# Optimization experiments

Hardware: AMD Instinct MI355X
Metric: run time of the kernel (lower is better)

The kernel has to match this reference:

```python
import jax, jax.numpy as jnp
import numpy as np
import math

D_MODEL = 1024
N_HEADS = 16
D_FF = 4096
D_K = D_MODEL // N_HEADS
B, S = 2, 2048
EPS = 1e-5


def _linear_params(key, fan_in, fan_out):
    kw, kb = jax.random.split(key)
    bound = 1.0 / math.sqrt(fan_in)
    W = jax.random.uniform(kw, (fan_out, fan_in), jnp.float32, -bound, bound)
    b = jax.random.uniform(kb, (fan_out,), jnp.float32, -bound, bound)
    return W, b


def setup_inputs() -> dict:
    key = jax.random.key(0)
    ks = jax.random.split(key, 8)
    x = jax.random.normal(ks[0], (B, S, D_MODEL), jnp.float32)
    # causal mask, broadcast over batch and heads; 0 -> masked
    mask = jnp.tril(jnp.ones((S, S), jnp.int32))[None, None, :, :]
    wq, bq = _linear_params(ks[1], D_MODEL, D_MODEL)
    wk, bk = _linear_params(ks[2], D_MODEL, D_MODEL)
    wv, bv = _linear_params(ks[3], D_MODEL, D_MODEL)
    wo, bo = _linear_params(ks[4], D_MODEL, D_MODEL)
    w1, b1 = _linear_params(ks[5], D_MODEL, D_FF)
    w2, b2 = _linear_params(ks[6], D_FF, D_MODEL)
    g1 = jnp.ones((D_MODEL,), jnp.float32)
    be1 = jnp.zeros((D_MODEL,), jnp.float32)
    g2 = jnp.ones((D_MODEL,), jnp.float32)
    be2 = jnp.zeros((D_MODEL,), jnp.float32)
    return dict(x=x, mask=mask, wq=wq, bq=bq, wk=wk, bk=bk, wv=wv, bv=bv,
                wo=wo, bo=bo, w1=w1, b1=b1, w2=w2, b2=b2,
                g1=g1, be1=be1, g2=g2, be2=be2)


def _layernorm(x, g, b):
    mu = jnp.mean(x, axis=-1, keepdims=True)
    var = jnp.mean(jnp.square(x - mu), axis=-1, keepdims=True)
    return (x - mu) * jax.lax.rsqrt(var + EPS) * g + b


def reference(x, mask, wq, bq, wk, bk, wv, bv, wo, bo, w1, b1, w2, b2, g1, be1, g2, be2):
    Bsz, Sl, _ = x.shape
    def heads(t):  # [B,S,D] -> [B,H,S,d_k]
        return t.reshape(Bsz, Sl, N_HEADS, D_K).transpose(0, 2, 1, 3)
    Q = heads(x @ wq.T + bq)
    K = heads(x @ wk.T + bk)
    V = heads(x @ wv.T + bv)
    scores = jnp.einsum('bhqd,bhkd->bhqk', Q, K) / math.sqrt(D_K)
    scores = jnp.where(mask == 0, jnp.float32(-1e9), scores)
    attn = jax.nn.softmax(scores, axis=-1)
    out = jnp.einsum('bhqk,bhkd->bhqd', attn, V)
    out = out.transpose(0, 2, 1, 3).reshape(Bsz, Sl, D_MODEL)
    attn_out = out @ wo.T + bo
    h = _layernorm(x + attn_out, g1, be1)  # dropout is identity in eval
    ff = jax.nn.relu(h @ w1.T + b1) @ w2.T + b2
    return _layernorm(h + ff, g2, be2)
```

## Files before the change

kernel.cpp:

```cpp
#include <hip/hip_runtime.h>
#include <hip/hip_bf16.h>


using f32x4 = __attribute__((ext_vector_type(4))) float;
using s16x8 = __attribute__((ext_vector_type(8))) short;

constexpr int D_MODEL = 1024;
constexpr int D_FF    = 4096;
constexpr int DK      = 64;
constexpr int BB      = 2;
constexpr int SS      = 2048;
constexpr int NTOK    = BB * SS;

#define QSCALE 0.18033688011112042f

__device__ __forceinline__ ushort f2bf(float f) {
    unsigned u = __float_as_uint(f);
    u += 0x7fffu + ((u >> 16) & 1u);
    return (ushort)(u >> 16);
}

__device__ __forceinline__ float bflo(uint v) { return __uint_as_float(v << 16); }
__device__ __forceinline__ float bfhi(uint v) { return __uint_as_float(v & 0xffff0000u); }

__device__ __forceinline__ float ex2(float x) {
    float r;
    asm("v_exp_f32 %0, %1" : "=v"(r) : "v"(x));
    return r;
}

__device__ __forceinline__ void gload_lds16(const void* g, void* l) {
    __builtin_amdgcn_global_load_lds(
        (const __attribute__((address_space(1))) void*)g,
        (__attribute__((address_space(3))) void*)l, 16, 0, 0);
}

__device__ __forceinline__ void wait_vm4() {
    asm volatile("s_waitcnt vmcnt(4)" ::: "memory");
    __builtin_amdgcn_sched_barrier(0);
}
__device__ __forceinline__ void wait_vm0() {
    asm volatile("s_waitcnt vmcnt(0)" ::: "memory");
    __builtin_amdgcn_sched_barrier(0);
}
__device__ __forceinline__ void wait_lgkm0() {
    asm volatile("s_waitcnt lgkmcnt(0)" ::: "memory");
    __builtin_amdgcn_sched_barrier(0);
}

struct CvtArgs { const float* src[7]; ushort* dst[7]; };

__global__ __launch_bounds__(256) void cvt_all(CvtArgs a) {
    constexpr long S[8] = {0L<<20, 1L<<20, 2L<<20, 3L<<20,
                           4L<<20, 8L<<20, 12L<<20, 16L<<20};
    long i = ((long)blockIdx.x * 256 + threadIdx.x) * 4;
    int s = 0;
#pragma unroll
    for (int j = 1; j < 7; ++j) if (i >= S[j]) s = j;
    long off = i - S[s];
    float4 v = *(const float4*)(a.src[s] + off);
    ushort4 o;
    o.x = f2bf(v.x); o.y = f2bf(v.y); o.z = f2bf(v.z); o.w = f2bf(v.w);
    *(ushort4*)(a.dst[s] + off) = o;
}

__global__ __launch_bounds__(512, 2) void gemm256_relu(
        const ushort* __restrict__ A, const ushort* __restrict__ Wt,
        const float* __restrict__ bias, ushort* __restrict__ C,
        int M, int N, int K) {
    __shared__ __align__(16) char Als[2][2][128 * 128];
    __shared__ __align__(16) char Bls[2][2][128 * 128];

    const int nwg = (int)gridDim.x;
    const int id  = (int)blockIdx.x;
    const int sw  = (id & 7) * (nwg >> 3) + (id >> 3);
    const int gx  = N >> 8;
    const int bx  = sw % gx, by = sw / gx;
    const int bm0 = by << 8, bn0 = bx << 8;

    const int t  = threadIdx.x;
    const int l  = t & 63;
    const int w  = t >> 6;
    const int li = l & 15, g = l >> 4;
    const int wm = w >> 2, wn = w & 3;

    const int srow  = w * 8 + (l >> 3);
    const int scolb = (l & 7) * 16;
    const int svz   = (scolb ^ ((srow & 7) << 4)) >> 1;
    const int nk    = K >> 6;

    auto stA = [&](int buf, int half, int kt) {
        if (kt >= nk) return;
        const ushort* src = A + (size_t)(bm0 + half * 128 + srow) * K + kt * 64 + svz;
        char* dst = Als[buf][half] + w * 1024;
        gload_lds16(src, dst);
        gload_lds16(src + (size_t)64 * K, dst + 8192);
    };
    auto stB = [&](int buf, int half, int kt) {
        if (kt >= nk) return;
        const ushort* src = Wt + (size_t)(bn0 + half * 128 + srow) * K + kt * 64 + svz;
        char* dst = Bls[buf][half] + w * 1024;
        gload_lds16(src, dst);
        gload_lds16(src + (size_t)64 * K, dst + 8192);
    };

    const int rdsw = (li & 7) << 4;

    f32x4 acc[8][4];
#pragma unroll
    for (int m = 0; m < 8; ++m)
#pragma unroll
        for (int n = 0; n < 4; ++n)
            acc[m][n] = (f32x4){0.f, 0.f, 0.f, 0.f};

    auto ldA2 = [&](int buf, int q, s16x8 af[2][2]) {
#pragma unroll
        for (int m2 = 0; m2 < 2; ++m2)
#pragma unroll
            for (int kk = 0; kk < 2; ++kk)
                af[m2][kk] = *(const s16x8*)(Als[buf][wm] +
                    ((q * 2 + m2) * 16 + li) * 128 + ((kk * 64 + g * 16) ^ rdsw));
    };
    auto ldB8 = [&](int buf, s16x8 bfr[4][2]) {
#pragma unroll
        for (int nf = 0; nf < 4; ++nf)
#pragma unroll
            for (int kk = 0; kk < 2; ++kk)
                bfr[nf][kk] = *(const s16x8*)(Bls[buf][wn >> 1] +
                    ((wn & 1) * 64 + nf * 16 + li) * 128 + ((kk * 64 + g * 16) ^ rdsw));
    };
    auto mfmaq = [&](int q, s16x8 af[2][2], s16x8 bfr[4][2], int wm_mode) {
        __builtin_amdgcn_s_barrier();
        wait_lgkm0();
        __builtin_amdgcn_s_setprio(1);
#pragma unroll
        for (int m2 = 0; m2 < 2; ++m2)
#pragma unroll
            for (int nf = 0; nf < 4; ++nf)
#pragma unroll
            for (int kk = 0; kk < 2; ++kk)
                acc[q * 2 + m2][nf] = __builtin_amdgcn_mfma_f32_16x16x32_bf16(
                    af[m2][kk], bfr[nf][kk], acc[q * 2 + m2][nf], 0, 0, 0);
        __builtin_amdgcn_s_setprio(0);
        if (wm_mode == 4) wait_vm4();
        else if (wm_mode == 0) wait_vm0();
        __builtin_amdgcn_s_barrier();
    };

    stB(0, 0, 0); stB(0, 1, 0);
    stA(0, 0, 0); stA(0, 1, 0);
    stB(1, 0, 1); stB(1, 1, 1);
    wait_vm4();
    __builtin_amdgcn_s_barrier();

    const int ni = nk >> 1;
    for (int i = 0; i < ni; ++i) {
        const int t0 = 2 * i;
        const bool last = (i == ni - 1);
        {
            s16x8 bfr[4][2];
            { ldB8(0, bfr); s16x8 af[2][2]; ldA2(0, 0, af);
              stA(1, 0, t0 + 1);                      mfmaq(0, af, bfr, -1); }
            { s16x8 af[2][2]; ldA2(0, 1, af);
              stA(1, 1, t0 + 1); stB(0, 0, t0 + 2);   mfmaq(1, af, bfr, -1); }
            { s16x8 af[2][2]; ldA2(0, 2, af);
              stB(0, 1, t0 + 2);                      mfmaq(2, af, bfr, -1); }
            { s16x8 af[2][2]; ldA2(0, 3, af);
                                                      mfmaq(3, af, bfr, last ? 0 : 4); }
        }
        {
            s16x8 bfr[4][2];
            { ldB8(1, bfr); s16x8 af[2][2]; ldA2(1, 0, af);
              stA(0, 0, t0 + 2);                      mfmaq(0, af, bfr, -1); }
            { s16x8 af[2][2]; ldA2(1, 1, af);
              stA(0, 1, t0 + 2);                      mfmaq(1, af, bfr, -1); }
            { s16x8 af[2][2]; ldA2(1, 2, af);
              stB(1, 0, t0 + 3);                      mfmaq(2, af, bfr, -1); }
            { s16x8 af[2][2]; ldA2(1, 3, af);
              stB(1, 1, t0 + 3);
                                                      mfmaq(3, af, bfr, last ? -1 : 4); }
        }
    }

#pragma unroll
    for (int mf = 0; mf < 8; ++mf) {
        int row0 = bm0 + wm * 128 + mf * 16 + g * 4;
#pragma unroll
        for (int nf = 0; nf < 4; ++nf) {
            int col = bn0 + wn * 64 + nf * 16 + li;
            float bsv = bias[col];
#pragma unroll
            for (int r = 0; r < 4; ++r) {
                float v = fmaxf(acc[mf][nf][r] + bsv, 0.f);
                C[(size_t)(row0 + r) * N + col] = f2bf(v);
            }
        }
    }
}

__global__ __launch_bounds__(512, 2) void gemm256_qkvt(
        const ushort* __restrict__ xb, const ushort* __restrict__ wqkb,
        const ushort* __restrict__ wvb,
        const float* __restrict__ bq, const float* __restrict__ bk,
        const float* __restrict__ bv,
        ushort* __restrict__ QKb, ushort* __restrict__ VtG) {
    __shared__ __align__(16) char Als[2][2][128 * 128];
    __shared__ __align__(16) char Bls[2][2][128 * 128];

    const int id = (int)blockIdx.x;
    const int sw = (id & 7) * 24 + (id >> 3);
    const bool vt = (sw >= 128);
    const ushort *Aop, *Wop;
    int bm0, bn0;
    if (!vt) { bm0 = (sw >> 3) << 8;  bn0 = (sw & 7) << 8;          Aop = xb;  Wop = wqkb; }
    else     { int s2 = sw - 128; bm0 = (s2 >> 4) << 8; bn0 = (s2 & 15) << 8; Aop = wvb; Wop = xb; }

    const int t  = threadIdx.x;
    const int l  = t & 63;
    const int w  = t >> 6;
    const int li = l & 15, g = l >> 4;
    const int wm = w >> 2, wn = w & 3;

    const int srow  = w * 8 + (l >> 3);
    const int scolb = (l & 7) * 16;
    const int svz   = (scolb ^ ((srow & 7) << 4)) >> 1;
    constexpr int K = 1024, nk = 16;

    auto stA = [&](int buf, int half, int kt) {
        if (kt >= nk) return;
        const ushort* src = Aop + (size_t)(bm0 + half * 128 + srow) * K + kt * 64 + svz;
        char* dst = Als[buf][half] + w * 1024;
        gload_lds16(src, dst);
        gload_lds16(src + (size_t)64 * K, dst + 8192);
    };
    auto stB = [&](int buf, int half, int kt) {
        if (kt >= nk) return;
        const ushort* src = Wop + (size_t)(bn0 + half * 128 + srow) * K + kt * 64 + svz;
        char* dst = Bls[buf][half] + w * 1024;
        gload_lds16(src, dst);
        gload_lds16(src + (size_t)64 * K, dst + 8192);
    };

    const int rdsw = (li & 7) << 4;

    f32x4 acc[8][4];
#pragma unroll
    for (int m = 0; m < 8; ++m)
#pragma unroll
        for (int n = 0; n < 4; ++n)
            acc[m][n] = (f32x4){0.f, 0.f, 0.f, 0.f};

    auto ldA2 = [&](int buf, int q, s16x8 af[2][2]) {
#pragma unroll
        for (int m2 = 0; m2 < 2; ++m2)
#pragma unroll
            for (int kk = 0; kk < 2; ++kk)
                af[m2][kk] = *(const s16x8*)(Als[buf][wm] +
                    ((q * 2 + m2) * 16 + li) * 128 + ((kk * 64 + g * 16) ^ rdsw));
    };
    auto ldB8 = [&](int buf, s16x8 bfr[4][2]) {
#pragma unroll
        for (int nf = 0; nf < 4; ++nf)
#pragma unroll
            for (int kk = 0; kk < 2; ++kk)
                bfr[nf][kk] = *(const s16x8*)(Bls[buf][wn >> 1] +
                    ((wn & 1) * 64 + nf * 16 + li) * 128 + ((kk * 64 + g * 16) ^ rdsw));
    };
    auto mfmaq = [&](int q, s16x8 af[2][2], s16x8 bfr[4][2], int wm_mode) {
        __builtin_amdgcn_s_barrier();
        wait_lgkm0();
        __builtin_amdgcn_s_setprio(1);
#pragma unroll
        for (int m2 = 0; m2 < 2; ++m2)
#pragma unroll
            for (int nf = 0; nf < 4; ++nf)
#pragma unroll
            for (int kk = 0; kk < 2; ++kk)
                acc[q * 2 + m2][nf] = __builtin_amdgcn_mfma_f32_16x16x32_bf16(
                    af[m2][kk], bfr[nf][kk], acc[q * 2 + m2][nf], 0, 0, 0);
        __builtin_amdgcn_s_setprio(0);
        if (wm_mode == 4) wait_vm4();
        else if (wm_mode == 0) wait_vm0();
        __builtin_amdgcn_s_barrier();
    };

    stB(0, 0, 0); stB(0, 1, 0);
    stA(0, 0, 0); stA(0, 1, 0);
    stB(1, 0, 1); stB(1, 1, 1);
    wait_vm4();
    __builtin_amdgcn_s_barrier();

    const int ni = nk >> 1;
    for (int i = 0; i < ni; ++i) {
        const int t0 = 2 * i;
        const bool last = (i == ni - 1);
        {
            s16x8 bfr[4][2];
            { ldB8(0, bfr); s16x8 af[2][2]; ldA2(0, 0, af);
              stA(1, 0, t0 + 1);                      mfmaq(0, af, bfr, -1); }
            { s16x8 af[2][2]; ldA2(0, 1, af);
              stA(1, 1, t0 + 1); stB(0, 0, t0 + 2);   mfmaq(1, af, bfr, -1); }
            { s16x8 af[2][2]; ldA2(0, 2, af);
              stB(0, 1, t0 + 2);                      mfmaq(2, af, bfr, -1); }
            { s16x8 af[2][2]; ldA2(0, 3, af);
                                                      mfmaq(3, af, bfr, last ? 0 : 4); }
        }
        {
            s16x8 bfr[4][2];
            { ldB8(1, bfr); s16x8 af[2][2]; ldA2(1, 0, af);
              stA(0, 0, t0 + 2);                      mfmaq(0, af, bfr, -1); }
            { s16x8 af[2][2]; ldA2(1, 1, af);
              stA(0, 1, t0 + 2);                      mfmaq(1, af, bfr, -1); }
            { s16x8 af[2][2]; ldA2(1, 2, af);
              stB(1, 0, t0 + 3);                      mfmaq(2, af, bfr, -1); }
            { s16x8 af[2][2]; ldA2(1, 3, af);
              stB(1, 1, t0 + 3);
                                                      mfmaq(3, af, bfr, last ? -1 : 4); }
        }
    }

#pragma unroll
    for (int mf = 0; mf < 8; ++mf) {
        int row0 = bm0 + wm * 128 + mf * 16 + g * 4;
#pragma unroll
        for (int nf = 0; nf < 4; ++nf) {
            int col = bn0 + wn * 64 + nf * 16 + li;
            if (!vt) {
                float bsv = (col < 1024) ? bq[col] : bk[col - 1024];
                float sc  = (col < 1024) ? QSCALE : 1.f;
#pragma unroll
                for (int r = 0; r < 4; ++r) {
                    float v = (acc[mf][nf][r] + bsv) * sc;
                    QKb[(size_t)(row0 + r) * 2048 + col] = f2bf(v);
                }
            } else {
#pragma unroll
                for (int r = 0; r < 4; ++r) {
                    float v = acc[mf][nf][r] + bv[row0 + r];
                    VtG[(size_t)(row0 + r) * 4096 + col] = f2bf(v);
                }
            }
        }
    }
}

__global__ __launch_bounds__(256, 2) void gemm_bt(
        const ushort* __restrict__ A, const ushort* __restrict__ W,
        const float* __restrict__ bias,
        ushort* __restrict__ Cout, int M, int N, int Klen, int ldk, int gx, int splitk) {
    __shared__ __align__(16) char Asb[2][128 * 128];
    __shared__ __align__(16) char Bsb[2][128 * 128];

    const int nwg = (int)gridDim.x;
    const int id  = (int)blockIdx.x;
    const int sw  = (id & 7) * (nwg >> 3) + (id >> 3);
    const int tps = nwg / splitk;
    const int s   = sw / tps;
    const int rem = sw - s * tps;
    const int bx  = rem % gx, by = rem / gx;

    const int t  = threadIdx.x;
    const int l  = t & 63;
    const int w  = t >> 6;
    const int wr = w >> 1, wc = w & 1;
    const int li = l & 15, g = l >> 4;
    const int bm0 = by << 7;
    const int bn0 = bx << 7;
    const int kbase = s * Klen;

    f32x4 acc[4][4];
#pragma unroll
    for (int m = 0; m < 4; ++m)
#pragma unroll
        for (int n = 0; n < 4; ++n)
            acc[m][n] = (f32x4){0.f, 0.f, 0.f, 0.f};

    const int rsub = l >> 3, slot = l & 7;
    const int swzel = (((slot * 16) ^ (rsub << 4)) >> 1);

    auto stage = [&](int buf, int k0) {
#pragma unroll
        for (int i = 0; i < 4; ++i) {
            const int rbase = i * 32 + w * 8;
            gload_lds16(A + (size_t)(bm0 + rbase + rsub) * ldk + kbase + k0 + swzel,
                        Asb[buf] + rbase * 128);
            gload_lds16(W + (size_t)(bn0 + rbase + rsub) * ldk + kbase + k0 + swzel,
                        Bsb[buf] + rbase * 128);
        }
    };

    const int nk = Klen >> 6;
    stage(0, 0);
    __syncthreads();

    for (int tt = 0; tt < nk; ++tt) {
        const int cur = tt & 1;
        if (tt + 1 < nk) stage(cur ^ 1, (tt + 1) << 6);
#pragma unroll
        for (int ks = 0; ks < 2; ++ks) {
            s16x8 af[4], bfr[4];
#pragma unroll
            for (int m = 0; m < 4; ++m) {
                int row = wr * 64 + m * 16 + li;
                af[m] = *(const s16x8*)(Asb[cur] + row * 128 + (((ks * 4 + g) * 16) ^ ((row & 7) << 4)));
            }
#pragma unroll
            for (int n = 0; n < 4; ++n) {
                int row = wc * 64 + n * 16 + li;
                bfr[n] = *(const s16x8*)(Bsb[cur] + row * 128 + (((ks * 4 + g) * 16) ^ ((row & 7) << 4)));
            }
            __builtin_amdgcn_s_setprio(1);
#pragma unroll
            for (int m = 0; m < 4; ++m)
#pragma unroll
                for (int n = 0; n < 4; ++n)
                    acc[m][n] = __builtin_amdgcn_mfma_f32_16x16x32_bf16(af[m], bfr[n], acc[m][n], 0, 0, 0);
            __builtin_amdgcn_s_setprio(0);
        }
        __syncthreads();
    }

    const bool dobias = (s == 0);
    ushort* Cb = Cout + (size_t)s * M * N;
#pragma unroll
    for (int m = 0; m < 4; ++m) {
        int row0 = bm0 + wr * 64 + m * 16 + g * 4;
#pragma unroll
        for (int n = 0; n < 4; ++n) {
            int col = bn0 + wc * 64 + n * 16 + li;
            float bsv = dobias ? bias[col] : 0.f;
#pragma unroll
            for (int r = 0; r < 4; ++r) {
                float v = acc[m][n][r] + bsv;
                Cb[(size_t)(row0 + r) * N + col] = f2bf(v);
            }
        }
    }
}

__global__ __launch_bounds__(256, 4) void attn_kernel(
        const ushort* __restrict__ QKb, const ushort* __restrict__ VtG,
        ushort* __restrict__ po, float* __restrict__ ml) {
    __shared__ __align__(16) char Ks[2][64 * 128];
    __shared__ __align__(16) char Vs[2][64 * 128];
    __shared__ __align__(16) char Ps[4][16 * 128];

    const int t  = threadIdx.x;
    const int l  = t & 63;
    const int w  = t >> 6;
    const int li = l & 15, g = l >> 4;

    const int id   = (int)blockIdx.x;
    const int xcd  = id & 7;
    const int rest = id >> 3;
    const int grp  = xcd + 8 * (rest >> 5);
    const int k32  = rest & 31;
    const int h    = grp >> 1;
    const int b    = grp & 1;
    const int bx   = k32 & 15;
    const int half = k32 >> 4;

    const ushort* Kp = QKb + (size_t)(b * SS) * 2048 + 1024 + h * DK;
    const ushort* Vp = VtG + (size_t)(h * DK) * NTOK + b * SS;

    const int rsub = l >> 3, slot = l & 7;
    const int swzsrc = (slot * 16) ^ (rsub << 4);

    auto stage = [&](int buf, int kt) {
#pragma unroll
        for (int c = 0; c < 2; ++c) {
            int row0 = (w + c * 4) * 8;
            gload_lds16((const char*)(Kp + (size_t)(kt + row0 + rsub) * 2048) + swzsrc,
                        Ks[buf] + row0 * 128);
            gload_lds16((const char*)(Vp + (size_t)(row0 + rsub) * NTOK + kt) + swzsrc,
                        Vs[buf] + row0 * 128);
        }
    };

    char* Pw = Ps[w];
    const int rswz = (li & 7) << 4;

    s16x8 vones;
#pragma unroll
    for (int j = 0; j < 8; ++j) vones[j] = (short)0x3F80;

    const int hi  = SS / 64 - 1 - bx;
    const int lo  = bx;
    const int qwH = hi * 64 + w * 16;
    const int qwL = lo * 64 + w * 16;

    s16x8 qfH[2], qfL[2];
    {
        const ushort* QpH = QKb + (size_t)(b * SS + qwH) * 2048 + h * DK;
        const ushort* QpL = QKb + (size_t)(b * SS + qwL) * 2048 + h * DK;
#pragma unroll
        for (int ds = 0; ds < 2; ++ds) {
            qfH[ds] = *(const s16x8*)(QpH + li * 2048 + ds * 32 + g * 8);
            qfL[ds] = *(const s16x8*)(QpL + li * 2048 + ds * 32 + g * 8);
        }
    }

    f32x4 oH[4], oL[4], osH, osL;
#pragma unroll
    for (int d = 0; d < 4; ++d) {
        oH[d] = (f32x4){0.f, 0.f, 0.f, 0.f};
        oL[d] = (f32x4){0.f, 0.f, 0.f, 0.f};
    }
    osH = (f32x4){0.f, 0.f, 0.f, 0.f};
    osL = (f32x4){0.f, 0.f, 0.f, 0.f};

    auto process = [&](const s16x8 (&qf)[2], f32x4 (&o)[4], f32x4& osum,
                       int j, int stripe, int qw, int cur) {
        const int kt = j * 64;
        f32x4 sa[4];
#pragma unroll
        for (int ks = 0; ks < 4; ++ks) sa[ks] = (f32x4){0.f, 0.f, 0.f, 0.f};
#pragma unroll
        for (int ks = 0; ks < 4; ++ks) {
            int row = ks * 16 + li;
#pragma unroll
            for (int ds = 0; ds < 2; ++ds) {
                s16x8 kf = *(const s16x8*)(Ks[cur] + row * 128 + ((ds * 64 + g * 16) ^ rswz));
                __builtin_amdgcn_s_setprio(1);
                sa[ks] = __builtin_amdgcn_mfma_f32_16x16x32_bf16(kf, qf[ds], sa[ks], 0, 0, 0);
                __builtin_amdgcn_s_setprio(0);
            }
        }

        const bool maskt = (j == stripe);
        float p[4][4];
#pragma unroll
        for (int ks = 0; ks < 4; ++ks)
#pragma unroll
            for (int r = 0; r < 4; ++r) {
                float sv = sa[ks][r];
                if (maskt && (kt + ks * 16 + g * 4 + r > qw + li)) sv = -1e30f;
                p[ks][r] = ex2(sv);
            }

#pragma unroll
        for (int ks = 0; ks < 4; ++ks) {
            uint u0, u1;
            asm("v_cvt_pk_bf16_f32 %0, %1, %2" : "=v"(u0) : "v"(p[ks][0]), "v"(p[ks][1]));
            asm("v_cvt_pk_bf16_f32 %0, %1, %2" : "=v"(u1) : "v"(p[ks][2]), "v"(p[ks][3]));
            uint2 uv; uv.x = u0; uv.y = u1;
            *(uint2*)(Pw + li * 128 + ((ks * 32 + g * 8) ^ rswz)) = uv;
        }

        s16x8 pf[2];
#pragma unroll
        for (int ks2 = 0; ks2 < 2; ++ks2)
            pf[ks2] = *(const s16x8*)(Pw + li * 128 + ((ks2 * 64 + g * 16) ^ rswz));
#pragma unroll
        for (int dblk = 0; dblk < 4; ++dblk) {
            int vrow = dblk * 16 + li;
#pragma unroll
            for (int ks2 = 0; ks2 < 2; ++ks2) {
                s16x8 vf = *(const s16x8*)(Vs[cur] + vrow * 128 + ((ks2 * 64 + g * 16) ^ rswz));
                __builtin_amdgcn_s_setprio(1);
                o[dblk] = __builtin_amdgcn_mfma_f32_16x16x32_bf16(pf[ks2], vf, o[dblk], 0, 0, 0);
                __builtin_amdgcn_s_setprio(0);
            }
        }
#pragma unroll
        for (int ks2 = 0; ks2 < 2; ++ks2)
            osum = __builtin_amdgcn_mfma_f32_16x16x32_bf16(pf[ks2], vones, osum, 0, 0, 0);
    };

    const int nt = ((hi - half) >> 1) + 1;
    stage(0, half * 64);
    __syncthreads();

    for (int it = 0; it < nt; ++it) {
        const int j   = half + 2 * it;
        const int cur = it & 1;
        if (it + 1 < nt) stage(cur ^ 1, j * 64 + 128);

        process(qfH, oH, osH, j, hi, qwH, cur);
        if (j <= lo)
            process(qfL, oL, osL, j, lo, qwL, cur);

        __syncthreads();
    }

#pragma unroll
    for (int r = 0; r < 4; ++r) {
        ushort* ppH = po + ((((size_t)(half * 2 + b)) * SS + qwH + g * 4 + r) * 16 + h) * 64;
        ushort* ppL = po + ((((size_t)(half * 2 + b)) * SS + qwL + g * 4 + r) * 16 + h) * 64;
#pragma unroll
        for (int dblk = 0; dblk < 4; ++dblk) {
            ppH[dblk * 16 + li] = f2bf(oH[dblk][r]);
            ppL[dblk * 16 + li] = f2bf(oL[dblk][r]);
        }
    }
    {
        const int qrow = l & 15;
        const int src  = (qrow >> 2) << 4;
        float tH0 = __shfl(osH[0], src), tH1 = __shfl(osH[1], src);
        float tH2 = __shfl(osH[2], src), tH3 = __shfl(osH[3], src);
        float tL0 = __shfl(osL[0], src), tL1 = __shfl(osL[1], src);
        float tL2 = __shfl(osL[2], src), tL3 = __shfl(osL[3], src);
        const int rr = qrow & 3;
        float lsH = rr == 0 ? tH0 : rr == 1 ? tH1 : rr == 2 ? tH2 : tH3;
        float lsL = rr == 0 ? tL0 : rr == 1 ? tL1 : rr == 2 ? tL2 : tL3;
        if (l < 16) {
            size_t mrowH = (((size_t)(half * 2 + b)) * SS + qwH + l) * 16 + h;
            ml[mrowH * 2]     = 0.f;
            ml[mrowH * 2 + 1] = lsH;
            size_t mrowL = (((size_t)(half * 2 + b)) * SS + qwL + l) * 16 + h;
            ml[mrowL * 2]     = 0.f;
            ml[mrowL * 2 + 1] = lsL;
        }
    }
}

__global__ __launch_bounds__(256) void attn_combine(
        const ushort* __restrict__ po, const float* __restrict__ ml,
        ushort* __restrict__ ctx) {
    const int idx = blockIdx.x * 256 + threadIdx.x;
    const int row = idx >> 4;
    const int d4  = (idx & 15) * 4;
    const int HR  = 2 * SS * 16;

    float m0 = ml[(size_t)row * 2],        l0 = ml[(size_t)row * 2 + 1];
    float m1 = ml[(size_t)(HR + row) * 2], l1 = ml[(size_t)(HR + row) * 2 + 1];
    float mx = fmaxf(m0, m1);
    float w0 = ex2(m0 - mx), w1 = ex2(m1 - mx);
    float inv = 1.0f / (l0 * w0 + l1 * w1);

    uint2 a = *(const uint2*)(po + (size_t)row * 64 + d4);
    uint2 c = *(const uint2*)(po + (size_t)(HR + row) * 64 + d4);
    float v0 = (bflo(a.x) * w0 + bflo(c.x) * w1) * inv;
    float v1 = (bfhi(a.x) * w0 + bfhi(c.x) * w1) * inv;
    float v2 = (bflo(a.y) * w0 + bflo(c.y) * w1) * inv;
    float v3 = (bfhi(a.y) * w0 + bfhi(c.y) * w1) * inv;
    ushort4 o;
    o.x = f2bf(v0); o.y = f2bf(v1); o.z = f2bf(v2); o.w = f2bf(v3);
    *(ushort4*)(ctx + (size_t)(row >> 4) * 1024 + (row & 15) * 64 + d4) = o;
}

template <bool WBF>
__global__ __launch_bounds__(256) void ln_fused(
        const float* __restrict__ xa, const ushort* __restrict__ pb,
        const float* __restrict__ gamma, const float* __restrict__ beta,
        float* __restrict__ outf, ushort* __restrict__ outb) {
    const int row = blockIdx.x;
    const int t   = threadIdx.x;
    const size_t off = (size_t)row * D_MODEL + t * 4;
    float4 a = *(const float4*)(xa + off);
    uint2 c = *(const uint2*)(pb + off);
    uint2 d = *(const uint2*)(pb + (size_t)NTOK * D_MODEL + off);
    float z0 = a.x + bflo(c.x) + bflo(d.x);
    float z1 = a.y + bfhi(c.x) + bfhi(d.x);
    float z2 = a.z + bflo(c.y) + bflo(d.y);
    float z3 = a.w + bfhi(c.y) + bfhi(d.y);
    float sum = z0 + z1 + z2 + z3;
    float sq  = z0 * z0 + z1 * z1 + z2 * z2 + z3 * z3;
#pragma unroll
    for (int o = 1; o < 64; o <<= 1) {
        sum += __shfl_xor(sum, o);
        sq  += __shfl_xor(sq, o);
    }
    __shared__ float s1[4], s2[4];
    if ((t & 63) == 0) { s1[t >> 6] = sum; s2[t >> 6] = sq; }
    __syncthreads();
    float tot = s1[0] + s1[1] + s1[2] + s1[3];
    float tsq = s2[0] + s2[1] + s2[2] + s2[3];
    const float invn = 1.0f / (float)D_MODEL;
    float mu  = tot * invn;
    float var = tsq * invn - mu * mu;
    float rstd = rsqrtf(var + 1e-5f);
    float4 gv = *(const float4*)(gamma + t * 4);
    float4 bv = *(const float4*)(beta + t * 4);
    float y0 = (z0 - mu) * rstd * gv.x + bv.x;
    float y1 = (z1 - mu) * rstd * gv.y + bv.y;
    float y2 = (z2 - mu) * rstd * gv.z + bv.z;
    float y3 = (z3 - mu) * rstd * gv.w + bv.w;
    float4 y = {y0, y1, y2, y3};
    *(float4*)(outf + off) = y;
    if constexpr (WBF) {
        ushort4 u;
        u.x = f2bf(y0); u.y = f2bf(y1); u.z = f2bf(y2); u.w = f2bf(y3);
        *(ushort4*)(outb + off) = u;
    }
}

extern "C" void kernel_launch(void* const* d_in, const int* in_sizes, int n_in,
                              void* d_out, int out_size, void* d_ws, size_t ws_size,
                              hipStream_t stream) {
    const float* x   = (const float*)d_in[0];
    const float* wq  = (const float*)d_in[2];  const float* bq  = (const float*)d_in[3];
    const float* wk  = (const float*)d_in[4];  const float* bk  = (const float*)d_in[5];
    const float* wv  = (const float*)d_in[6];  const float* bv  = (const float*)d_in[7];
    const float* wo  = (const float*)d_in[8];  const float* bo  = (const float*)d_in[9];
    const float* w1  = (const float*)d_in[10]; const float* b1  = (const float*)d_in[11];
    const float* w2  = (const float*)d_in[12]; const float* b2  = (const float*)d_in[13];
    const float* g1  = (const float*)d_in[14]; const float* be1 = (const float*)d_in[15];
    const float* g2  = (const float*)d_in[16]; const float* be2 = (const float*)d_in[17];
    float* out = (float*)d_out;

    char* ws = (char*)d_ws;
    const size_t MB = 1u << 20;
    ushort* wqkb = (ushort*)(ws + 0 * MB);
    ushort* wvb  = (ushort*)(ws + 4 * MB);
    ushort* wob  = (ushort*)(ws + 6 * MB);
    ushort* w1b  = (ushort*)(ws + 8 * MB);
    ushort* w2b  = (ushort*)(ws + 16 * MB);
    ushort* xb   = (ushort*)(ws + 24 * MB);
    ushort* QKb  = (ushort*)(ws + 32 * MB);
    ushort* VtG  = (ushort*)(ws + 48 * MB);
    ushort* ctx  = (ushort*)(ws + 56 * MB);
    ushort* po   = (ushort*)(ws + 64 * MB);
    float*  ml   = (float*)(ws + 81 * MB);
    ushort* p01  = (ushort*)(ws + 64 * MB);
    float*  h    = (float*)(ws + 96 * MB);
    ushort* hb   = (ushort*)(ws + 112 * MB);
    ushort* ffib = (ushort*)(ws + 24 * MB);

    CvtArgs ca;
    ca.src[0] = wq; ca.dst[0] = wqkb;
    ca.src[1] = wk; ca.dst[1] = wqkb + D_MODEL * D_MODEL;
    ca.src[2] = wv; ca.dst[2] = wvb;
    ca.src[3] = wo; ca.dst[3] = wob;
    ca.src[4] = w1; ca.dst[4] = w1b;
    ca.src[5] = w2; ca.dst[5] = w2b;
    ca.src[6] = x;  ca.dst[6] = xb;
    cvt_all<<<dim3(16384), dim3(256), 0, stream>>>(ca);

    gemm256_qkvt<<<dim3(192), dim3(512), 0, stream>>>(
        xb, wqkb, wvb, bq, bk, bv, QKb, VtG);

    attn_kernel<<<dim3(1024), dim3(256), 0, stream>>>(QKb, VtG, po, ml);
    attn_combine<<<dim3(4096), dim3(256), 0, stream>>>(po, ml, ctx);

    gemm_bt<<<dim3(512), dim3(256), 0, stream>>>(
        ctx, wob, bo, p01, NTOK, D_MODEL, 512, D_MODEL, 8, 2);
    ln_fused<true><<<dim3(NTOK), dim3(256), 0, stream>>>(x, p01, g1, be1, h, hb);

    gemm256_relu<<<dim3(256), dim3(512), 0, stream>>>(hb, w1b, b1, ffib, NTOK, D_FF, D_MODEL);

    gemm_bt<<<dim3(512), dim3(256), 0, stream>>>(
        ffib, w2b, b2, p01, NTOK, D_MODEL, 2048, D_FF, 8, 2);
    ln_fused<false><<<dim3(NTOK), dim3(256), 0, stream>>>(h, p01, g2, be2, out, nullptr);
}
```

Before: 213.1 us.

## Use pipelined 256x256 split-K GEMM for output and FFN-down projections

Replaces the 128x128 double-buffered gemm_bt with a generalized version of the 256x256, 512-thread software-pipelined GEMM already used for QKV. It now runs with split-K of 4, and the layernorm kernels sum four bf16 partial buffers instead of two. The larger tile with interleaved loads and MFMAs is meant to raise data reuse and keep the matrix units busier on the Wo and W2 projections. In exchange it doubles the partial-sum write and read traffic, which needs a workspace big enough for four partial buffers. The short K per split on the Wo GEMM also leaves little of the pipeline to work with.

```diff
diff --git a/kernel.cpp b/kernel.cpp
--- a/kernel.cpp
+++ b/kernel.cpp
@@ -198,22 +198,23 @@
     }
 }
 
-__global__ __launch_bounds__(512, 2) void gemm256_qkvt(
-        const ushort* __restrict__ xb, const ushort* __restrict__ wqkb,
-        const ushort* __restrict__ wvb,
-        const float* __restrict__ bq, const float* __restrict__ bk,
-        const float* __restrict__ bv,
-        ushort* __restrict__ QKb, ushort* __restrict__ VtG) {
+__global__ __launch_bounds__(512, 2) void gemm256_psum(
+        const ushort* __restrict__ A, const ushort* __restrict__ Wt,
+        const float* __restrict__ bias, ushort* __restrict__ Cout,
+        int M, int N, int Klen, int ldk, int splitk) {
     __shared__ __align__(16) char Als[2][2][128 * 128];
     __shared__ __align__(16) char Bls[2][2][128 * 128];
 
-    const int id = (int)blockIdx.x;
-    const int sw = (id & 7) * 24 + (id >> 3);
-    const bool vt = (sw >= 128);
-    const ushort *Aop, *Wop;
-    int bm0, bn0;
-    if (!vt) { bm0 = (sw >> 3) << 8;  bn0 = (sw & 7) << 8;          Aop = xb;  Wop = wqkb; }
-    else     { int s2 = sw - 128; bm0 = (s2 >> 4) << 8; bn0 = (s2 & 15) << 8; Aop = wvb; Wop = xb; }
+    const int nwg = (int)gridDim.x;
+    const int id  = (int)blockIdx.x;
+    const int sw  = (id & 7) * (nwg >> 3) + (id >> 3);
+    const int gx  = N >> 8;
+    const int tps = nwg / splitk;
+    const int s   = sw / tps;
+    const int rem = sw - s * tps;
+    const int bx  = rem % gx, by = rem / gx;
+    const int bm0 = by << 8, bn0 = bx << 8;
+    const int kbase = s * Klen;
 
     const int t  = threadIdx.x;
     const int l  = t & 63;
@@ -224,21 +225,21 @@
     const int srow  = w * 8 + (l >> 3);
     const int scolb = (l & 7) * 16;
     const int svz   = (scolb ^ ((srow & 7) << 4)) >> 1;
-    constexpr int K = 1024, nk = 16;
+    const int nk    = Klen >> 6;
 
     auto stA = [&](int buf, int half, int kt) {
         if (kt >= nk) return;
-        const ushort* src = Aop + (size_t)(bm0 + half * 128 + srow) * K + kt * 64 + svz;
+        const ushort* src = A + (size_t)(bm0 + half * 128 + srow) * ldk + kbase + kt * 64 + svz;
         char* dst = Als[buf][half] + w * 1024;
         gload_lds16(src, dst);
-        gload_lds16(src + (size_t)64 * K, dst + 8192);
+        gload_lds16(src + (size_t)64 * ldk, dst + 8192);
     };
     auto stB = [&](int buf, int half, int kt) {
         if (kt >= nk) return;
-        const ushort* src = Wop + (size_t)(bn0 + half * 128 + srow) * K + kt * 64 + svz;
+        const ushort* src = Wt + (size_t)(bn0 + half * 128 + srow) * ldk + kbase + kt * 64 + svz;
         char* dst = Bls[buf][half] + w * 1024;
         gload_lds16(src, dst);
-        gload_lds16(src + (size_t)64 * K, dst + 8192);
+        gload_lds16(src + (size_t)64 * ldk, dst + 8192);
     };
 
     const int rdsw = (li & 7) << 4;
@@ -319,6 +320,145 @@
         }
     }
 
+    const bool dobias = (s == 0);
+    ushort* Cb = Cout + (size_t)s * M * N;
+#pragma unroll
+    for (int mf = 0; mf < 8; ++mf) {
+        int row0 = bm0 + wm * 128 + mf * 16 + g * 4;
+#pragma unroll
+        for (int nf = 0; nf < 4; ++nf) {
+            int col = bn0 + wn * 64 + nf * 16 + li;
+            float bsv = dobias ? bias[col] : 0.f;
+#pragma unroll
+            for (int r = 0; r < 4; ++r) {
+                float v = acc[mf][nf][r] + bsv;
+                Cb[(size_t)(row0 + r) * N + col] = f2bf(v);
+            }
+        }
+    }
+}
+
+__global__ __launch_bounds__(512, 2) void gemm256_qkvt(
+        const ushort* __restrict__ xb, const ushort* __restrict__ wqkb,
+        const ushort* __restrict__ wvb,
+        const float* __restrict__ bq, const float* __restrict__ bk,
+        const float* __restrict__ bv,
+        ushort* __restrict__ QKb, ushort* __restrict__ VtG) {
+    __shared__ __align__(16) char Als[2][2][128 * 128];
+    __shared__ __align__(16) char Bls[2][2][128 * 128];
+
+    const int id = (int)blockIdx.x;
+    const int sw = (id & 7) * 24 + (id >> 3);
+    const bool vt = (sw >= 128);
+    const ushort *Aop, *Wop;
+    int bm0, bn0;
+    if (!vt) { bm0 = (sw >> 3) << 8;  bn0 = (sw & 7) << 8;          Aop = xb;  Wop = wqkb; }
+    else     { int s2 = sw - 128; bm0 = (s2 >> 4) << 8; bn0 = (s2 & 15) << 8; Aop = wvb; Wop = xb; }
+
+    const int t  = threadIdx.x;
+    const int l  = t & 63;
+    const int w  = t >> 6;
+    const int li = l & 15, g = l >> 4;
+    const int wm = w >> 2, wn = w & 3;
+
+    const int srow  = w * 8 + (l >> 3);
+    const int scolb = (l & 7) * 16;
+    const int svz   = (scolb ^ ((srow & 7) << 4)) >> 1;
+    constexpr int K = 1024, nk = 16;
+
+    auto stA = [&](int buf, int half, int kt) {
+        if (kt >= nk) return;
+        const ushort* src = Aop + (size_t)(bm0 + half * 128 + srow) * K + kt * 64 + svz;
+        char* dst = Als[buf][half] + w * 1024;
+        gload_lds16(src, dst);
+        gload_lds16(src + (size_t)64 * K, dst + 8192);
+    };
+    auto stB = [&](int buf, int half, int kt) {
+        if (kt >= nk) return;
+        const ushort* src = Wop + (size_t)(bn0 + half * 128 + srow) * K + kt * 64 + svz;
+        char* dst = Bls[buf][half] + w * 1024;
+        gload_lds16(src, dst);
+        gload_lds16(src + (size_t)64 * K, dst + 8192);
+    };
+
+    const int rdsw = (li & 7) << 4;
+
+    f32x4 acc[8][4];
+#pragma unroll
+    for (int m = 0; m < 8; ++m)
+#pragma unroll
+        for (int n = 0; n < 4; ++n)
+            acc[m][n] = (f32x4){0.f, 0.f, 0.f, 0.f};
+
+    auto ldA2 = [&](int buf, int q, s16x8 af[2][2]) {
+#pragma unroll
+        for (int m2 = 0; m2 < 2; ++m2)
+#pragma unroll
+            for (int kk = 0; kk < 2; ++kk)
+                af[m2][kk] = *(const s16x8*)(Als[buf][wm] +
+                    ((q * 2 + m2) * 16 + li) * 128 + ((kk * 64 + g * 16) ^ rdsw));
+    };
+    auto ldB8 = [&](int buf, s16x8 bfr[4][2]) {
+#pragma unroll
+        for (int nf = 0; nf < 4; ++nf)
+#pragma unroll
+            for (int kk = 0; kk < 2; ++kk)
+                bfr[nf][kk] = *(const s16x8*)(Bls[buf][wn >> 1] +
+                    ((wn & 1) * 64 + nf * 16 + li) * 128 + ((kk * 64 + g * 16) ^ rdsw));
+    };
+    auto mfmaq = [&](int q, s16x8 af[2][2], s16x8 bfr[4][2], int wm_mode) {
+        __builtin_amdgcn_s_barrier();
+        wait_lgkm0();
+        __builtin_amdgcn_s_setprio(1);
+#pragma unroll
+        for (int m2 = 0; m2 < 2; ++m2)
+#pragma unroll
+            for (int nf = 0; nf < 4; ++nf)
+#pragma unroll
+            for (int kk = 0; kk < 2; ++kk)
+                acc[q * 2 + m2][nf] = __builtin_amdgcn_mfma_f32_16x16x32_bf16(
+                    af[m2][kk], bfr[nf][kk], acc[q * 2 + m2][nf], 0, 0, 0);
+        __builtin_amdgcn_s_setprio(0);
+        if (wm_mode == 4) wait_vm4();
+        else if (wm_mode == 0) wait_vm0();
+        __builtin_amdgcn_s_barrier();
+    };
+
+    stB(0, 0, 0); stB(0, 1, 0);
+    stA(0, 0, 0); stA(0, 1, 0);
+    stB(1, 0, 1); stB(1, 1, 1);
+    wait_vm4();
+    __builtin_amdgcn_s_barrier();
+
+    const int ni = nk >> 1;
+    for (int i = 0; i < ni; ++i) {
+        const int t0 = 2 * i;
+        const bool last = (i == ni - 1);
+        {
+            s16x8 bfr[4][2];
+            { ldB8(0, bfr); s16x8 af[2][2]; ldA2(0, 0, af);
+              stA(1, 0, t0 + 1);                      mfmaq(0, af, bfr, -1); }
+            { s16x8 af[2][2]; ldA2(0, 1, af);
+              stA(1, 1, t0 + 1); stB(0, 0, t0 + 2);   mfmaq(1, af, bfr, -1); }
+            { s16x8 af[2][2]; ldA2(0, 2, af);
+              stB(0, 1, t0 + 2);                      mfmaq(2, af, bfr, -1); }
+            { s16x8 af[2][2]; ldA2(0, 3, af);
+                                                      mfmaq(3, af, bfr, last ? 0 : 4); }
+        }
+        {
+            s16x8 bfr[4][2];
+            { ldB8(1, bfr); s16x8 af[2][2]; ldA2(1, 0, af);
+              stA(0, 0, t0 + 2);                      mfmaq(0, af, bfr, -1); }
+            { s16x8 af[2][2]; ldA2(1, 1, af);
+              stA(0, 1, t0 + 2);                      mfmaq(1, af, bfr, -1); }
+            { s16x8 af[2][2]; ldA2(1, 2, af);
+              stB(1, 0, t0 + 3);                      mfmaq(2, af, bfr, -1); }
+            { s16x8 af[2][2]; ldA2(1, 3, af);
+              stB(1, 1, t0 + 3);
+                                                      mfmaq(3, af, bfr, last ? -1 : 4); }
+        }
+    }
+
 #pragma unroll
     for (int mf = 0; mf < 8; ++mf) {
         int row0 = bm0 + wm * 128 + mf * 16 + g * 4;
@@ -339,100 +479,6 @@
                     float v = acc[mf][nf][r] + bv[row0 + r];
                     VtG[(size_t)(row0 + r) * 4096 + col] = f2bf(v);
                 }
-            }
-        }
-    }
-}
-
-__global__ __launch_bounds__(256, 2) void gemm_bt(
-        const ushort* __restrict__ A, const ushort* __restrict__ W,
-        const float* __restrict__ bias,
-        ushort* __restrict__ Cout, int M, int N, int Klen, int ldk, int gx, int splitk) {
-    __shared__ __align__(16) char Asb[2][128 * 128];
-    __shared__ __align__(16) char Bsb[2][128 * 128];
-
-    const int nwg = (int)gridDim.x;
-    const int id  = (int)blockIdx.x;
-    const int sw  = (id & 7) * (nwg >> 3) + (id >> 3);
-    const int tps = nwg / splitk;
-    const int s   = sw / tps;
-    const int rem = sw - s * tps;
-    const int bx  = rem % gx, by = rem / gx;
-
-    const int t  = threadIdx.x;
-    const int l  = t & 63;
-    const int w  = t >> 6;
-    const int wr = w >> 1, wc = w & 1;
-    const int li = l & 15, g = l >> 4;
-    const int bm0 = by << 7;
-    const int bn0 = bx << 7;
-    const int kbase = s * Klen;
-
-    f32x4 acc[4][4];
-#pragma unroll
-    for (int m = 0; m < 4; ++m)
-#pragma unroll
-        for (int n = 0; n < 4; ++n)
-            acc[m][n] = (f32x4){0.f, 0.f, 0.f, 0.f};
-
-    const int rsub = l >> 3, slot = l & 7;
-    const int swzel = (((slot * 16) ^ (rsub << 4)) >> 1);
-
-    auto stage = [&](int buf, int k0) {
-#pragma unroll
-        for (int i = 0; i < 4; ++i) {
-            const int rbase = i * 32 + w * 8;
-            gload_lds16(A + (size_t)(bm0 + rbase + rsub) * ldk + kbase + k0 + swzel,
-                        Asb[buf] + rbase * 128);
-            gload_lds16(W + (size_t)(bn0 + rbase + rsub) * ldk + kbase + k0 + swzel,
-                        Bsb[buf] + rbase * 128);
-        }
-    };
-
-    const int nk = Klen >> 6;
-    stage(0, 0);
-    __syncthreads();
-
-    for (int tt = 0; tt < nk; ++tt) {
-        const int cur = tt & 1;
-        if (tt + 1 < nk) stage(cur ^ 1, (tt + 1) << 6);
-#pragma unroll
-        for (int ks = 0; ks < 2; ++ks) {
-            s16x8 af[4], bfr[4];
-#pragma unroll
-            for (int m = 0; m < 4; ++m) {
-                int row = wr * 64 + m * 16 + li;
-                af[m] = *(const s16x8*)(Asb[cur] + row * 128 + (((ks * 4 + g) * 16) ^ ((row & 7) << 4)));
-            }
-#pragma unroll
-            for (int n = 0; n < 4; ++n) {
-                int row = wc * 64 + n * 16 + li;
-                bfr[n] = *(const s16x8*)(Bsb[cur] + row * 128 + (((ks * 4 + g) * 16) ^ ((row & 7) << 4)));
-            }
-            __builtin_amdgcn_s_setprio(1);
-#pragma unroll
-            for (int m = 0; m < 4; ++m)
-#pragma unroll
-                for (int n = 0; n < 4; ++n)
-                    acc[m][n] = __builtin_amdgcn_mfma_f32_16x16x32_bf16(af[m], bfr[n], acc[m][n], 0, 0, 0);
-            __builtin_amdgcn_s_setprio(0);
-        }
-        __syncthreads();
-    }
-
-    const bool dobias = (s == 0);
-    ushort* Cb = Cout + (size_t)s * M * N;
-#pragma unroll
-    for (int m = 0; m < 4; ++m) {
-        int row0 = bm0 + wr * 64 + m * 16 + g * 4;
-#pragma unroll
-        for (int n = 0; n < 4; ++n) {
-            int col = bn0 + wc * 64 + n * 16 + li;
-            float bsv = dobias ? bias[col] : 0.f;
-#pragma unroll
-            for (int r = 0; r < 4; ++r) {
-                float v = acc[m][n][r] + bsv;
-                Cb[(size_t)(row0 + r) * N + col] = f2bf(v);
             }
         }
     }
@@ -648,12 +694,12 @@
     const int t   = threadIdx.x;
     const size_t off = (size_t)row * D_MODEL + t * 4;
     float4 a = *(const float4*)(xa + off);
-    uint2 c = *(const uint2*)(pb + off);
-    uint2 d = *(const uint2*)(pb + (size_t)NTOK * D_MODEL + off);
-    float z0 = a.x + bflo(c.x) + bflo(d.x);
-    float z1 = a.y + bfhi(c.x) + bfhi(d.x);
-    float z2 = a.z + bflo(c.y) + bflo(d.y);
-    float z3 = a.w + bfhi(c.y) + bfhi(d.y);
+    float z0 = a.x, z1 = a.y, z2 = a.z, z3 = a.w;
+#pragma unroll
+    for (int s = 0; s < 4; ++s) {
+        uint2 c = *(const uint2*)(pb + (size_t)s * NTOK * D_MODEL + off);
+        z0 += bflo(c.x); z1 += bfhi(c.x); z2 += bflo(c.y); z3 += bfhi(c.y);
+    }
     float sum = z0 + z1 + z2 + z3;
     float sq  = z0 * z0 + z1 * z1 + z2 * z2 + z3 * z3;
 #pragma unroll
@@ -733,13 +779,13 @@
     attn_kernel<<<dim3(1024), dim3(256), 0, stream>>>(QKb, VtG, po, ml);
     attn_combine<<<dim3(4096), dim3(256), 0, stream>>>(po, ml, ctx);
 
-    gemm_bt<<<dim3(512), dim3(256), 0, stream>>>(
-        ctx, wob, bo, p01, NTOK, D_MODEL, 512, D_MODEL, 8, 2);
+    gemm256_psum<<<dim3(256), dim3(512), 0, stream>>>(
+        ctx, wob, bo, p01, NTOK, D_MODEL, 256, D_MODEL, 4);
     ln_fused<true><<<dim3(NTOK), dim3(256), 0, stream>>>(x, p01, g1, be1, h, hb);
 
     gemm256_relu<<<dim3(256), dim3(512), 0, stream>>>(hb, w1b, b1, ffib, NTOK, D_FF, D_MODEL);
 
-    gemm_bt<<<dim3(512), dim3(256), 0, stream>>>(
-        ffib, w2b, b2, p01, NTOK, D_MODEL, 2048, D_FF, 8, 2);
+    gemm256_psum<<<dim3(256), dim3(512), 0, stream>>>(
+        ffib, w2b, b2, p01, NTOK, D_MODEL, 1024, D_FF, 4);
     ln_fused<false><<<dim3(NTOK), dim3(256), 0, stream>>>(h, p01, g2, be2, out, nullptr);
 }
```

Result: no change. 216.1 us (+1.4%).
